# Optimization experiments

Hardware: AMD Instinct MI355X
Metric: run time of the kernel (lower is better)

Reference implementation:

```python
import jax, jax.numpy as jnp
import numpy as np

E = 512      # embed_dim
H = 8        # num_heads
HD = E // H  # head_dim
TGT = 512
SRC = 2048
B = 16


def setup_inputs() -> dict:
    key = jax.random.key(0)
    ks = jax.random.split(key, 10)
    inp = {
        "query": jax.random.normal(ks[0], (TGT, B, E), dtype=jnp.float32),
        "key": jax.random.normal(ks[1], (SRC, B, E), dtype=jnp.float32),
        "value": jax.random.normal(ks[2], (SRC, B, E), dtype=jnp.float32),
        "in_proj_weight": jax.random.normal(ks[3], (3 * E, E), dtype=jnp.float32) * 0.02,
        "in_proj_bias": jax.random.normal(ks[4], (3 * E,), dtype=jnp.float32) * 0.02,
        "bias_k": jax.random.normal(ks[5], (1, 1, E), dtype=jnp.float32) * 0.02,
        "bias_v": jax.random.normal(ks[6], (1, 1, E), dtype=jnp.float32) * 0.02,
        "out_proj_weight": jax.random.normal(ks[7], (E, E), dtype=jnp.float32) * 0.02,
        "out_proj_bias": jnp.zeros((E,), dtype=jnp.float32),
        "key_padding_mask": jax.random.randint(ks[8], (B, SRC), 0, 2).astype(bool),
    }
    return inp


def reference(query, key, value, in_proj_weight, in_proj_bias, bias_k, bias_v,
              out_proj_weight, out_proj_bias, key_padding_mask):
    tgt_len, bsz, embed_dim = query.shape
    scaling = float(HD) ** -0.5

    # manual in-projection (query != key, key is value -> separate q, fused kv)
    q = query @ in_proj_weight[:E].T + in_proj_bias[:E]
    k = key @ in_proj_weight[E:2 * E].T + in_proj_bias[E:2 * E]
    v = value @ in_proj_weight[2 * E:].T + in_proj_bias[2 * E:]
    q = q * scaling

    # bias_k / bias_v concatenation along src dim; pad key_padding_mask with False
    k = jnp.concatenate([k, jnp.broadcast_to(bias_k, (1, bsz, E))], axis=0)
    v = jnp.concatenate([v, jnp.broadcast_to(bias_v, (1, bsz, E))], axis=0)
    kpm = jnp.pad(key_padding_mask, ((0, 0), (0, 1)))  # [B, SRC+1]

    src_len = k.shape[0]
    # [len, B, E] -> [B*H, len, HD]
    q = q.reshape(tgt_len, bsz * H, HD).transpose(1, 0, 2)
    k = k.reshape(src_len, bsz * H, HD).transpose(1, 0, 2)
    v = v.reshape(src_len, bsz * H, HD).transpose(1, 0, 2)

    scores = jnp.einsum('bth,bsh->bts', q, k)  # [B*H, TGT, SRC+1]
    mask = kpm[:, None, None, :]               # [B, 1, 1, SRC+1]
    scores = scores.reshape(bsz, H, tgt_len, src_len)
    scores = jnp.where(mask, -jnp.inf, scores).reshape(bsz * H, tgt_len, src_len)
    attn = jax.nn.softmax(scores, axis=-1)

    out = jnp.einsum('bts,bsh->bth', attn, v)                 # [B*H, TGT, HD]
    out = out.transpose(1, 0, 2).reshape(tgt_len, bsz, E)     # [TGT, B, E]
    out = out @ out_proj_weight.T + out_proj_bias
    return out, attn
```

## Files before the change

### kernel.cpp

```cpp
#include <hip/hip_runtime.h>

#define E    512
#define H    8
#define HD   64
#define TGT  512
#define SRC  2048
#define S1   2049
#define S1P  2112
#define NB   16
#define BH   128
#define NCH  33
#define PW   2120

typedef __attribute__((ext_vector_type(8))) short short8;
typedef __attribute__((ext_vector_type(4))) float floatx4;

__device__ __forceinline__ unsigned short f2bf(float x) {
    unsigned u = __float_as_uint(x);
    u = (u + 0x7FFF + ((u >> 16) & 1)) >> 16;
    return (unsigned short)u;
}

__global__ __launch_bounds__(256) void cvt_bf16(const float* __restrict__ src,
    unsigned short* __restrict__ dst, const int n8)
{
    const int i = blockIdx.x * 256 + threadIdx.x;
    if (i >= n8) return;
    const float4 f0 = ((const float4*)src)[(size_t)i * 2];
    const float4 f1 = ((const float4*)src)[(size_t)i * 2 + 1];
    unsigned short o[8] = {f2bf(f0.x), f2bf(f0.y), f2bf(f0.z), f2bf(f0.w),
                           f2bf(f1.x), f2bf(f1.y), f2bf(f1.z), f2bf(f1.w)};
    ((int4*)dst)[i] = *(int4*)o;
}

__global__ __launch_bounds__(256) void proj_gemm(const unsigned short* __restrict__ X,
    const unsigned short* __restrict__ W, const float* __restrict__ bias,
    unsigned short* __restrict__ Y, const int ld, const float scale)
{
    __shared__ __align__(16) unsigned short As[128][72];
    __shared__ __align__(16) unsigned short Bs[64][72];
    const int tid  = threadIdx.x;
    const int c0   = blockIdx.x << 6;
    const int r0   = blockIdx.y << 7;
    const int w    = tid >> 6, lane = tid & 63, c = lane & 15, quad = lane >> 4;
    floatx4 acc[2][4] = {};
    for (int k0 = 0; k0 < E; k0 += 64) {
#pragma unroll
        for (int i = 0; i < 4; ++i) {
            const int idx = tid + (i << 8);
            const int r = idx >> 3, q = (idx & 7) << 3;
            *(int4*)&As[r][q] = *(const int4*)&X[(size_t)(r0 + r) * E + k0 + q];
        }
#pragma unroll
        for (int i = 0; i < 2; ++i) {
            const int idx = tid + (i << 8);
            const int r = idx >> 3, q = (idx & 7) << 3;
            *(int4*)&Bs[r][q] = *(const int4*)&W[(size_t)(c0 + r) * E + k0 + q];
        }
        __syncthreads();
#pragma unroll
        for (int kh = 0; kh < 2; ++kh) {
            short8 a0 = *(const short8*)&As[(w << 5) + c][(kh << 5) + (quad << 3)];
            short8 a1 = *(const short8*)&As[(w << 5) + 16 + c][(kh << 5) + (quad << 3)];
#pragma unroll
            for (int n = 0; n < 4; ++n) {
                short8 b = *(const short8*)&Bs[(n << 4) + c][(kh << 5) + (quad << 3)];
                acc[0][n] = __builtin_amdgcn_mfma_f32_16x16x32_bf16(a0, b, acc[0][n], 0, 0, 0);
                acc[1][n] = __builtin_amdgcn_mfma_f32_16x16x32_bf16(a1, b, acc[1][n], 0, 0, 0);
            }
        }
        __syncthreads();
    }
#pragma unroll
    for (int mt = 0; mt < 2; ++mt) {
#pragma unroll
        for (int reg = 0; reg < 4; ++reg) {
            const int rg = r0 + (w << 5) + (mt << 4) + (quad << 2) + reg;
            const int t = rg >> 4, b = rg & 15;
#pragma unroll
            for (int n = 0; n < 4; ++n) {
                const int col = c0 + (n << 4) + c;
                const int h = col >> 6, hd = col & 63;
                const float v = (acc[mt][n][reg] + bias[col]) * scale;
                Y[((size_t)(b * H + h) * ld + t) * HD + hd] = f2bf(v);
            }
        }
    }
}

__global__ void fill_bias(const float* __restrict__ bk, const float* __restrict__ bv,
                          unsigned short* __restrict__ kbuf, unsigned short* __restrict__ vtbuf)
{
    const int idx = blockIdx.x * 256 + threadIdx.x;
    const int bh = idx >> 6, hd = idx & 63, h = bh & 7;
    kbuf[((size_t)bh * S1P + SRC) * HD + hd] = f2bf(bk[h * HD + hd]);
    vtbuf[((size_t)bh * HD + hd) * S1P + SRC] = f2bf(bv[h * HD + hd]);
    for (int s = SRC + 1; s < S1P; ++s) {
        kbuf[((size_t)bh * S1P + s) * HD + hd] = 0;
        vtbuf[((size_t)bh * HD + hd) * S1P + s] = 0;
    }
}

__global__ __launch_bounds__(256) void transpose_v(const unsigned short* __restrict__ vbuf,
    unsigned short* __restrict__ vtbuf)
{
    __shared__ __align__(16) unsigned short T[64][72];
    const int tid = threadIdx.x;
    const int s0  = blockIdx.x << 6;
    const int bh  = blockIdx.y;
#pragma unroll
    for (int i = 0; i < 2; ++i) {
        const int idx = tid + (i << 8);
        const int s = idx >> 3, q = (idx & 7) << 3;
        *(int4*)&T[s][q] = *(const int4*)&vbuf[((size_t)bh * SRC + s0 + s) * HD + q];
    }
    __syncthreads();
#pragma unroll
    for (int i = 0; i < 2; ++i) {
        const int idx = tid + (i << 8);
        const int hd = idx >> 3, sq = (idx & 7) << 3;
        unsigned short tmp[8];
#pragma unroll
        for (int j = 0; j < 8; ++j) tmp[j] = T[sq + j][hd];
        *(int4*)&vtbuf[((size_t)bh * HD + hd) * S1P + s0 + sq] = *(int4*)tmp;
    }
}

__global__ __launch_bounds__(256, 2) void attn_fused(
    const unsigned short* __restrict__ qbh,
    const unsigned short* __restrict__ kbuf,
    const unsigned short* __restrict__ vtbuf,
    const int* __restrict__ kpm,
    float* __restrict__ attn, unsigned short* __restrict__ ctx)
{
    __shared__ __align__(16) unsigned short P[16][PW];
    __shared__ float mf[S1P];
    __shared__ float sums[4][16];
    __shared__ float linv[16];
    const int tid = threadIdx.x;
    const int t0  = blockIdx.x << 4;
    const int bh  = blockIdx.y;
    const int bb  = bh >> 3;
    const int w = tid >> 6, lane = tid & 63, c = lane & 15, quad = lane >> 4;

    for (int s = tid; s < S1P; s += 256)
        mf[s] = (s < SRC) ? (kpm[bb * SRC + s] ? 3e38f : 0.f)
                          : ((s == SRC) ? 0.f : 3e38f);

    const unsigned short* qr = &qbh[((size_t)bh * TGT + t0 + c) * HD + (quad << 3)];
    short8 qa0 = *(const short8*)qr;
    short8 qa1 = *(const short8*)(qr + 32);

    __syncthreads();

    float rs[4] = {0.f, 0.f, 0.f, 0.f};
    for (int ch = w; ch < NCH; ch += 4) {
        const int s0 = ch << 6;
        floatx4 sc[4] = {};
#pragma unroll
        for (int n = 0; n < 4; ++n) {
            const unsigned short* kr =
                &kbuf[((size_t)bh * S1P + s0 + (n << 4) + c) * HD + (quad << 3)];
            short8 b0 = *(const short8*)kr;
            short8 b1 = *(const short8*)(kr + 32);
            sc[n] = __builtin_amdgcn_mfma_f32_16x16x32_bf16(qa0, b0, sc[n], 0, 0, 0);
            sc[n] = __builtin_amdgcn_mfma_f32_16x16x32_bf16(qa1, b1, sc[n], 0, 0, 0);
        }
#pragma unroll
        for (int n = 0; n < 4; ++n) {
            const float m = mf[s0 + (n << 4) + c];
#pragma unroll
            for (int reg = 0; reg < 4; ++reg) {
                const float p = __expf(sc[n][reg] - m);
                rs[reg] += p;
                P[(quad << 2) + reg][s0 + (n << 4) + c] = f2bf(p);
            }
        }
    }

#pragma unroll
    for (int reg = 0; reg < 4; ++reg) {
        float v = rs[reg];
        v += __shfl_xor(v, 1); v += __shfl_xor(v, 2);
        v += __shfl_xor(v, 4); v += __shfl_xor(v, 8);
        rs[reg] = v;
    }
    if (c == 0) {
#pragma unroll
        for (int reg = 0; reg < 4; ++reg)
            sums[w][(quad << 2) + reg] = rs[reg];
    }
    __syncthreads();
    if (tid < 16)
        linv[tid] = 1.0f / (sums[0][tid] + sums[1][tid] + sums[2][tid] + sums[3][tid]);
    __syncthreads();

    floatx4 ca = {};
#pragma unroll 6
    for (int kc = 0; kc < 66; ++kc) {
        short8 a = *(const short8*)&P[c][(kc << 5) + (quad << 3)];
        short8 b = *(const short8*)&vtbuf[((size_t)bh * HD + (w << 4) + c) * S1P
                                          + (kc << 5) + (quad << 3)];
        ca = __builtin_amdgcn_mfma_f32_16x16x32_bf16(a, b, ca, 0, 0, 0);
    }
#pragma unroll
    for (int reg = 0; reg < 4; ++reg) {
        const int t = t0 + (quad << 2) + reg;
        ctx[((size_t)bh * TGT + t) * HD + (w << 4) + c] =
            f2bf(ca[reg] * linv[(quad << 2) + reg]);
    }

    for (int ch = w; ch < NCH; ch += 4) {
        const int s0 = ch << 6;
        if (ch < 32) {
#pragma unroll
            for (int r = 0; r < 16; ++r) {
                const float p =
                    __uint_as_float((unsigned)P[r][s0 + lane] << 16) * linv[r];
                attn[((size_t)bh * TGT + t0 + r) * S1 + s0 + lane] = p;
            }
        } else if (lane < 16) {
            const float p =
                __uint_as_float((unsigned)P[lane][2048] << 16) * linv[lane];
            attn[((size_t)bh * TGT + t0 + lane) * S1 + 2048] = p;
        }
    }
}

__global__ __launch_bounds__(256) void outproj_gemm(const unsigned short* __restrict__ ctx,
    const unsigned short* __restrict__ W, const float* __restrict__ bias,
    float* __restrict__ out)
{
    __shared__ __align__(16) unsigned short As[128][72];
    __shared__ __align__(16) unsigned short Bs[64][72];
    const int tid = threadIdx.x;
    const int c0  = blockIdx.x << 6;
    const int r0  = blockIdx.y << 7;
    const int w   = tid >> 6, lane = tid & 63, c = lane & 15, quad = lane >> 4;
    floatx4 acc[2][4] = {};
    for (int k0 = 0; k0 < E; k0 += 64) {
        const int h = k0 >> 6;
#pragma unroll
        for (int i = 0; i < 4; ++i) {
            const int idx = tid + (i << 8);
            const int r = idx >> 3, q = (idx & 7) << 3;
            const int rg = r0 + r, t = rg >> 4, b = rg & 15;
            *(int4*)&As[r][q] = *(const int4*)&ctx[((size_t)(b * H + h) * TGT + t) * HD + q];
        }
#pragma unroll
        for (int i = 0; i < 2; ++i) {
            const int idx = tid + (i << 8);
            const int r = idx >> 3, q = (idx & 7) << 3;
            *(int4*)&Bs[r][q] = *(const int4*)&W[(size_t)(c0 + r) * E + k0 + q];
        }
        __syncthreads();
#pragma unroll
        for (int kh = 0; kh < 2; ++kh) {
            short8 a0 = *(const short8*)&As[(w << 5) + c][(kh << 5) + (quad << 3)];
            short8 a1 = *(const short8*)&As[(w << 5) + 16 + c][(kh << 5) + (quad << 3)];
#pragma unroll
            for (int n = 0; n < 4; ++n) {
                short8 b = *(const short8*)&Bs[(n << 4) + c][(kh << 5) + (quad << 3)];
                acc[0][n] = __builtin_amdgcn_mfma_f32_16x16x32_bf16(a0, b, acc[0][n], 0, 0, 0);
                acc[1][n] = __builtin_amdgcn_mfma_f32_16x16x32_bf16(a1, b, acc[1][n], 0, 0, 0);
            }
        }
        __syncthreads();
    }
#pragma unroll
    for (int mt = 0; mt < 2; ++mt) {
#pragma unroll
        for (int reg = 0; reg < 4; ++reg) {
            const int rg = r0 + (w << 5) + (mt << 4) + (quad << 2) + reg;
#pragma unroll
            for (int n = 0; n < 4; ++n) {
                const int col = c0 + (n << 4) + c;
                out[(size_t)rg * E + col] = acc[mt][n][reg] + bias[col];
            }
        }
    }
}

extern "C" void kernel_launch(void* const* d_in, const int* in_sizes, int n_in,
                              void* d_out, int out_size, void* d_ws, size_t ws_size,
                              hipStream_t stream)
{
    const float* query  = (const float*)d_in[0];
    const float* key    = (const float*)d_in[1];
    const float* value  = (const float*)d_in[2];
    const float* ipw    = (const float*)d_in[3];
    const float* ipb    = (const float*)d_in[4];
    const float* bias_k = (const float*)d_in[5];
    const float* bias_v = (const float*)d_in[6];
    const float* opw    = (const float*)d_in[7];
    const float* opb    = (const float*)d_in[8];
    const int*   kpm    = (const int*)d_in[9];

    float* out  = (float*)d_out;
    float* attn = out + (size_t)TGT * NB * E;

    unsigned short* k_bf = (unsigned short*)attn;
    unsigned short* v_bf = k_bf + (size_t)16777216;
    unsigned short* vbuf = v_bf + (size_t)16777216;

    char* ws = (char*)d_ws;
    unsigned short* q_bf  = (unsigned short*)ws;
    unsigned short* wi_bf = q_bf  + (size_t)4194304;
    unsigned short* wo_bf = wi_bf + (size_t)786432;
    unsigned short* qbh   = wo_bf + (size_t)262144;
    unsigned short* kbuf  = qbh   + (size_t)4194304;
    unsigned short* vtbuf = kbuf  + (size_t)17301504;
    unsigned short* ctx   = vtbuf + (size_t)17301504;

    cvt_bf16<<<dim3(2048), 256, 0, stream>>>(query, q_bf, 524288);
    cvt_bf16<<<dim3(8192), 256, 0, stream>>>(key,   k_bf, 2097152);
    cvt_bf16<<<dim3(8192), 256, 0, stream>>>(value, v_bf, 2097152);
    cvt_bf16<<<dim3(384),  256, 0, stream>>>(ipw,   wi_bf, 98304);
    cvt_bf16<<<dim3(128),  256, 0, stream>>>(opw,   wo_bf, 32768);

    proj_gemm<<<dim3(8, 64),  256, 0, stream>>>(q_bf, wi_bf,          ipb,         qbh,  TGT, 0.125f);
    proj_gemm<<<dim3(8, 256), 256, 0, stream>>>(k_bf, wi_bf + 262144, ipb + E,     kbuf, S1P, 1.0f);
    proj_gemm<<<dim3(8, 256), 256, 0, stream>>>(v_bf, wi_bf + 524288, ipb + 2 * E, vbuf, SRC, 1.0f);

    fill_bias<<<dim3(32), 256, 0, stream>>>(bias_k, bias_v, kbuf, vtbuf);
    transpose_v<<<dim3(32, 128), 256, 0, stream>>>(vbuf, vtbuf);

    attn_fused<<<dim3(32, 128), 256, 0, stream>>>(qbh, kbuf, vtbuf, kpm, attn, ctx);
    outproj_gemm<<<dim3(8, 64), 256, 0, stream>>>(ctx, wo_bf, opb, out);
}
```

Baseline: 1.106 ms.

## Software-pipeline K/V loads and overlap attn stores with PV MFMA

The QK loop now double-buffers K fragments in registers, loading the next chunk while the current one is computed. The PV loop is restructured to 64-wide steps with two accumulators and prefetched V fragments. The attention-probability stores, previously a separate pass, are interleaved into the PV loop and use nontemporal stores, as is the ctx write. The aim is to hide global-load latency and overlap the large attn write with MFMA work, at the cost of higher register pressure.

```diff
diff --git a/kernel.cpp b/kernel.cpp
--- a/kernel.cpp
+++ b/kernel.cpp
@@ -151,32 +151,51 @@
     short8 qa0 = *(const short8*)qr;
     short8 qa1 = *(const short8*)(qr + 32);
 
+#define LOADK(D0, D1, CH) do {                                                  \
+        const unsigned short* kb_ = &kbuf[((size_t)bh * S1P + ((CH) << 6)) * HD]; \
+        _Pragma("unroll")                                                       \
+        for (int n_ = 0; n_ < 4; ++n_) {                                        \
+            const unsigned short* kr_ = kb_ + ((n_ << 4) + c) * HD + (quad << 3); \
+            D0[n_] = *(const short8*)kr_;                                       \
+            D1[n_] = *(const short8*)(kr_ + 32);                                \
+        }                                                                       \
+    } while (0)
+
+#define QK_COMPUTE(CH, B0, B1) do {                                             \
+        const int s0_ = (CH) << 6;                                              \
+        floatx4 sc_[4] = {};                                                    \
+        _Pragma("unroll")                                                       \
+        for (int n_ = 0; n_ < 4; ++n_) {                                        \
+            sc_[n_] = __builtin_amdgcn_mfma_f32_16x16x32_bf16(qa0, B0[n_], sc_[n_], 0, 0, 0); \
+            sc_[n_] = __builtin_amdgcn_mfma_f32_16x16x32_bf16(qa1, B1[n_], sc_[n_], 0, 0, 0); \
+        }                                                                       \
+        _Pragma("unroll")                                                       \
+        for (int n_ = 0; n_ < 4; ++n_) {                                        \
+            const float m_ = mf[s0_ + (n_ << 4) + c];                           \
+            _Pragma("unroll")                                                   \
+            for (int rg_ = 0; rg_ < 4; ++rg_) {                                 \
+                const float p_ = __expf(sc_[n_][rg_] - m_);                     \
+                rs[rg_] += p_;                                                  \
+                P[(quad << 2) + rg_][s0_ + (n_ << 4) + c] = f2bf(p_);           \
+            }                                                                   \
+        }                                                                       \
+    } while (0)
+
+    short8 kb0[4], kb1[4];
+    LOADK(kb0, kb1, w);
+
     __syncthreads();
 
     float rs[4] = {0.f, 0.f, 0.f, 0.f};
-    for (int ch = w; ch < NCH; ch += 4) {
-        const int s0 = ch << 6;
-        floatx4 sc[4] = {};
-#pragma unroll
-        for (int n = 0; n < 4; ++n) {
-            const unsigned short* kr =
-                &kbuf[((size_t)bh * S1P + s0 + (n << 4) + c) * HD + (quad << 3)];
-            short8 b0 = *(const short8*)kr;
-            short8 b1 = *(const short8*)(kr + 32);
-            sc[n] = __builtin_amdgcn_mfma_f32_16x16x32_bf16(qa0, b0, sc[n], 0, 0, 0);
-            sc[n] = __builtin_amdgcn_mfma_f32_16x16x32_bf16(qa1, b1, sc[n], 0, 0, 0);
-        }
-#pragma unroll
-        for (int n = 0; n < 4; ++n) {
-            const float m = mf[s0 + (n << 4) + c];
-#pragma unroll
-            for (int reg = 0; reg < 4; ++reg) {
-                const float p = __expf(sc[n][reg] - m);
-                rs[reg] += p;
-                P[(quad << 2) + reg][s0 + (n << 4) + c] = f2bf(p);
-            }
-        }
-    }
+    int ch;
+    for (ch = w; ch + 4 < NCH; ch += 4) {
+        short8 nb0[4], nb1[4];
+        LOADK(nb0, nb1, ch + 4);
+        QK_COMPUTE(ch, kb0, kb1);
+#pragma unroll
+        for (int n = 0; n < 4; ++n) { kb0[n] = nb0[n]; kb1[n] = nb1[n]; }
+    }
+    QK_COMPUTE(ch, kb0, kb1);
 
 #pragma unroll
     for (int reg = 0; reg < 4; ++reg) {
@@ -195,36 +214,56 @@
         linv[tid] = 1.0f / (sums[0][tid] + sums[1][tid] + sums[2][tid] + sums[3][tid]);
     __syncthreads();
 
-    floatx4 ca = {};
-#pragma unroll 6
-    for (int kc = 0; kc < 66; ++kc) {
-        short8 a = *(const short8*)&P[c][(kc << 5) + (quad << 3)];
-        short8 b = *(const short8*)&vtbuf[((size_t)bh * HD + (w << 4) + c) * S1P
-                                          + (kc << 5) + (quad << 3)];
-        ca = __builtin_amdgcn_mfma_f32_16x16x32_bf16(a, b, ca, 0, 0, 0);
-    }
+#define STORE_CHUNK(CH) do {                                                    \
+        if ((CH) < 32) {                                                        \
+            _Pragma("unroll")                                                   \
+            for (int r_ = 0; r_ < 16; ++r_) {                                   \
+                const float p_ = __uint_as_float(                               \
+                    (unsigned)P[r_][((CH) << 6) + lane] << 16) * linv[r_];      \
+                __builtin_nontemporal_store(p_,                                 \
+                    &attn[((size_t)bh * TGT + t0 + r_) * S1 + ((CH) << 6) + lane]); \
+            }                                                                   \
+        } else if (lane < 16) {                                                 \
+            const float p_ = __uint_as_float(                                   \
+                (unsigned)P[lane][2048] << 16) * linv[lane];                    \
+            __builtin_nontemporal_store(p_,                                     \
+                &attn[((size_t)bh * TGT + t0 + lane) * S1 + 2048]);             \
+        }                                                                       \
+    } while (0)
+
+    const unsigned short* vrow = &vtbuf[((size_t)bh * HD + (w << 4) + c) * S1P];
+    floatx4 ca0 = {}, ca1 = {};
+    short8 vb0 = *(const short8*)&vrow[(quad << 3)];
+    short8 vb1 = *(const short8*)&vrow[32 + (quad << 3)];
+#pragma unroll 4
+    for (int kc = 0; kc < 32; ++kc) {
+        short8 nv0 = *(const short8*)&vrow[((kc + 1) << 6) + (quad << 3)];
+        short8 nv1 = *(const short8*)&vrow[((kc + 1) << 6) + 32 + (quad << 3)];
+        short8 a0 = *(const short8*)&P[c][(kc << 6) + (quad << 3)];
+        short8 a1 = *(const short8*)&P[c][(kc << 6) + 32 + (quad << 3)];
+        ca0 = __builtin_amdgcn_mfma_f32_16x16x32_bf16(a0, vb0, ca0, 0, 0, 0);
+        ca1 = __builtin_amdgcn_mfma_f32_16x16x32_bf16(a1, vb1, ca1, 0, 0, 0);
+        if ((kc & 3) == w) STORE_CHUNK(kc);
+        vb0 = nv0; vb1 = nv1;
+    }
+    {
+        short8 a0 = *(const short8*)&P[c][(32 << 6) + (quad << 3)];
+        short8 a1 = *(const short8*)&P[c][(32 << 6) + 32 + (quad << 3)];
+        ca0 = __builtin_amdgcn_mfma_f32_16x16x32_bf16(a0, vb0, ca0, 0, 0, 0);
+        ca1 = __builtin_amdgcn_mfma_f32_16x16x32_bf16(a1, vb1, ca1, 0, 0, 0);
+        if (w == 0) STORE_CHUNK(32);
+    }
+
 #pragma unroll
     for (int reg = 0; reg < 4; ++reg) {
         const int t = t0 + (quad << 2) + reg;
-        ctx[((size_t)bh * TGT + t) * HD + (w << 4) + c] =
-            f2bf(ca[reg] * linv[(quad << 2) + reg]);
-    }
-
-    for (int ch = w; ch < NCH; ch += 4) {
-        const int s0 = ch << 6;
-        if (ch < 32) {
-#pragma unroll
-            for (int r = 0; r < 16; ++r) {
-                const float p =
-                    __uint_as_float((unsigned)P[r][s0 + lane] << 16) * linv[r];
-                attn[((size_t)bh * TGT + t0 + r) * S1 + s0 + lane] = p;
-            }
-        } else if (lane < 16) {
-            const float p =
-                __uint_as_float((unsigned)P[lane][2048] << 16) * linv[lane];
-            attn[((size_t)bh * TGT + t0 + lane) * S1 + 2048] = p;
-        }
-    }
+        const float v = (ca0[reg] + ca1[reg]) * linv[(quad << 2) + reg];
+        __builtin_nontemporal_store(f2bf(v),
+            &ctx[((size_t)bh * TGT + t) * HD + (w << 4) + c]);
+    }
+#undef LOADK
+#undef QK_COMPUTE
+#undef STORE_CHUNK
 }
 
 __global__ __launch_bounds__(256) void outproj_gemm(const unsigned short* __restrict__ ctx,
```

New measurement: 1.094 ms. Within noise of the previous version (-1.1%).

## Widen attention block to 8 waves with prefetched K and split PV reduction

Applied to the files above, without the earlier changes.

The fused attention kernel now runs 512 threads per block. The QK loop software-prefetches the next K chunk and its mask values into registers, replacing the shared-memory mask table. The PV product is split across two halves of the source dimension and combined through shared memory, using two accumulators to raise MFMA independence. fill_bias is also rewritten to parallelise the zero-padding writes over many threads with vectorised stores. The launch bounds of (512,4) and the larger shared footprint may limit occupancy or force register spills.

```diff
diff --git a/kernel.cpp b/kernel.cpp
--- a/kernel.cpp
+++ b/kernel.cpp
@@ -88,15 +88,27 @@
     }
 }
 
-__global__ void fill_bias(const float* __restrict__ bk, const float* __restrict__ bv,
-                          unsigned short* __restrict__ kbuf, unsigned short* __restrict__ vtbuf)
+#define FB_BIAS  8192
+#define FB_KPAD  64512
+#define FB_VPAD  516096
+__global__ __launch_bounds__(256) void fill_bias(const float* __restrict__ bk,
+    const float* __restrict__ bv,
+    unsigned short* __restrict__ kbuf, unsigned short* __restrict__ vtbuf)
 {
     const int idx = blockIdx.x * 256 + threadIdx.x;
-    const int bh = idx >> 6, hd = idx & 63, h = bh & 7;
-    kbuf[((size_t)bh * S1P + SRC) * HD + hd] = f2bf(bk[h * HD + hd]);
-    vtbuf[((size_t)bh * HD + hd) * S1P + SRC] = f2bf(bv[h * HD + hd]);
-    for (int s = SRC + 1; s < S1P; ++s) {
-        kbuf[((size_t)bh * S1P + s) * HD + hd] = 0;
+    if (idx < FB_BIAS) {
+        const int bh = idx >> 6, hd = idx & 63, h = bh & 7;
+        kbuf[((size_t)bh * S1P + SRC) * HD + hd] = f2bf(bk[h * HD + hd]);
+        vtbuf[((size_t)bh * HD + hd) * S1P + SRC] = f2bf(bv[h * HD + hd]);
+    } else if (idx < FB_BIAS + FB_KPAD) {
+        const int i = idx - FB_BIAS;
+        const int bh = i / 504, o = i % 504;
+        const int4 z = {0, 0, 0, 0};
+        ((int4*)&kbuf[((size_t)bh * S1P + S1) * HD])[o] = z;
+    } else if (idx < FB_BIAS + FB_KPAD + FB_VPAD) {
+        const int i = idx - FB_BIAS - FB_KPAD;
+        const int bh = i / 4032, r = i % 4032;
+        const int hd = r / 63, s = S1 + r % 63;
         vtbuf[((size_t)bh * HD + hd) * S1P + s] = 0;
     }
 }
@@ -126,7 +138,7 @@
     }
 }
 
-__global__ __launch_bounds__(256, 2) void attn_fused(
+__global__ __launch_bounds__(512, 4) void attn_fused(
     const unsigned short* __restrict__ qbh,
     const unsigned short* __restrict__ kbuf,
     const unsigned short* __restrict__ vtbuf,
@@ -134,8 +146,8 @@
     float* __restrict__ attn, unsigned short* __restrict__ ctx)
 {
     __shared__ __align__(16) unsigned short P[16][PW];
-    __shared__ float mf[S1P];
-    __shared__ float sums[4][16];
+    __shared__ float cpart[16][68];
+    __shared__ float sums[8][16];
     __shared__ float linv[16];
     const int tid = threadIdx.x;
     const int t0  = blockIdx.x << 4;
@@ -143,40 +155,59 @@
     const int bb  = bh >> 3;
     const int w = tid >> 6, lane = tid & 63, c = lane & 15, quad = lane >> 4;
 
-    for (int s = tid; s < S1P; s += 256)
-        mf[s] = (s < SRC) ? (kpm[bb * SRC + s] ? 3e38f : 0.f)
-                          : ((s == SRC) ? 0.f : 3e38f);
-
     const unsigned short* qr = &qbh[((size_t)bh * TGT + t0 + c) * HD + (quad << 3)];
     short8 qa0 = *(const short8*)qr;
     short8 qa1 = *(const short8*)(qr + 32);
 
-    __syncthreads();
+#define LOADK(D0, D1, M, CH) do {                                               \
+        const unsigned short* kb_ = &kbuf[((size_t)bh * S1P + ((CH) << 6)) * HD]; \
+        _Pragma("unroll")                                                       \
+        for (int n_ = 0; n_ < 4; ++n_) {                                        \
+            const unsigned short* kr_ = kb_ + ((n_ << 4) + c) * HD + (quad << 3); \
+            D0[n_] = *(const short8*)kr_;                                       \
+            D1[n_] = *(const short8*)(kr_ + 32);                                \
+        }                                                                       \
+        _Pragma("unroll")                                                       \
+        for (int n_ = 0; n_ < 4; ++n_) {                                        \
+            const int s_ = ((CH) << 6) + (n_ << 4) + c;                         \
+            M[n_] = (s_ < SRC) ? (kpm[bb * SRC + s_] ? 3e38f : 0.f)             \
+                               : ((s_ == SRC) ? 0.f : 3e38f);                   \
+        }                                                                       \
+    } while (0)
+
+#define QK_COMPUTE(CH, B0, B1, M) do {                                          \
+        const int s0_ = (CH) << 6;                                              \
+        floatx4 sc_[4] = {};                                                    \
+        _Pragma("unroll")                                                       \
+        for (int n_ = 0; n_ < 4; ++n_) {                                        \
+            sc_[n_] = __builtin_amdgcn_mfma_f32_16x16x32_bf16(qa0, B0[n_], sc_[n_], 0, 0, 0); \
+            sc_[n_] = __builtin_amdgcn_mfma_f32_16x16x32_bf16(qa1, B1[n_], sc_[n_], 0, 0, 0); \
+        }                                                                       \
+        _Pragma("unroll")                                                       \
+        for (int n_ = 0; n_ < 4; ++n_) {                                        \
+            _Pragma("unroll")                                                   \
+            for (int rg_ = 0; rg_ < 4; ++rg_) {                                 \
+                const float p_ = __expf(sc_[n_][rg_] - M[n_]);                  \
+                rs[rg_] += p_;                                                  \
+                P[(quad << 2) + rg_][s0_ + (n_ << 4) + c] = f2bf(p_);           \
+            }                                                                   \
+        }                                                                       \
+    } while (0)
 
     float rs[4] = {0.f, 0.f, 0.f, 0.f};
-    for (int ch = w; ch < NCH; ch += 4) {
-        const int s0 = ch << 6;
-        floatx4 sc[4] = {};
-#pragma unroll
-        for (int n = 0; n < 4; ++n) {
-            const unsigned short* kr =
-                &kbuf[((size_t)bh * S1P + s0 + (n << 4) + c) * HD + (quad << 3)];
-            short8 b0 = *(const short8*)kr;
-            short8 b1 = *(const short8*)(kr + 32);
-            sc[n] = __builtin_amdgcn_mfma_f32_16x16x32_bf16(qa0, b0, sc[n], 0, 0, 0);
-            sc[n] = __builtin_amdgcn_mfma_f32_16x16x32_bf16(qa1, b1, sc[n], 0, 0, 0);
-        }
-#pragma unroll
-        for (int n = 0; n < 4; ++n) {
-            const float m = mf[s0 + (n << 4) + c];
-#pragma unroll
-            for (int reg = 0; reg < 4; ++reg) {
-                const float p = __expf(sc[n][reg] - m);
-                rs[reg] += p;
-                P[(quad << 2) + reg][s0 + (n << 4) + c] = f2bf(p);
-            }
-        }
-    }
+    short8 kb0[4], kb1[4];
+    float mk[4];
+    LOADK(kb0, kb1, mk, w);
+    int ch;
+    for (ch = w; ch + 8 < NCH; ch += 8) {
+        short8 nb0[4], nb1[4];
+        float nm[4];
+        LOADK(nb0, nb1, nm, ch + 8);
+        QK_COMPUTE(ch, kb0, kb1, mk);
+#pragma unroll
+        for (int n = 0; n < 4; ++n) { kb0[n] = nb0[n]; kb1[n] = nb1[n]; mk[n] = nm[n]; }
+    }
+    QK_COMPUTE(ch, kb0, kb1, mk);
 
 #pragma unroll
     for (int reg = 0; reg < 4; ++reg) {
@@ -191,28 +222,51 @@
             sums[w][(quad << 2) + reg] = rs[reg];
     }
     __syncthreads();
-    if (tid < 16)
-        linv[tid] = 1.0f / (sums[0][tid] + sums[1][tid] + sums[2][tid] + sums[3][tid]);
+    if (tid < 16) {
+        float s = 0.f;
+#pragma unroll
+        for (int i = 0; i < 8; ++i) s += sums[i][tid];
+        linv[tid] = 1.0f / s;
+    }
     __syncthreads();
 
-    floatx4 ca = {};
-#pragma unroll 6
-    for (int kc = 0; kc < 66; ++kc) {
-        short8 a = *(const short8*)&P[c][(kc << 5) + (quad << 3)];
-        short8 b = *(const short8*)&vtbuf[((size_t)bh * HD + (w << 4) + c) * S1P
-                                          + (kc << 5) + (quad << 3)];
-        ca = __builtin_amdgcn_mfma_f32_16x16x32_bf16(a, b, ca, 0, 0, 0);
-    }
-#pragma unroll
-    for (int reg = 0; reg < 4; ++reg) {
-        const int t = t0 + (quad << 2) + reg;
-        ctx[((size_t)bh * TGT + t) * HD + (w << 4) + c] =
-            f2bf(ca[reg] * linv[(quad << 2) + reg]);
-    }
-
-    for (int ch = w; ch < NCH; ch += 4) {
-        const int s0 = ch << 6;
-        if (ch < 32) {
+    const int hs = w & 3, kh2 = w >> 2;
+    const int base = kh2 * 1056;
+    const unsigned short* vrow = &vtbuf[((size_t)bh * HD + (hs << 4) + c) * S1P + base];
+    const unsigned short* prow = &P[c][base];
+    floatx4 ca0 = {}, ca1 = {};
+#pragma unroll 4
+    for (int kc = 0; kc < 16; ++kc) {
+        short8 a0 = *(const short8*)&prow[(kc << 6) + (quad << 3)];
+        short8 a1 = *(const short8*)&prow[(kc << 6) + 32 + (quad << 3)];
+        short8 b0 = *(const short8*)&vrow[(kc << 6) + (quad << 3)];
+        short8 b1 = *(const short8*)&vrow[(kc << 6) + 32 + (quad << 3)];
+        ca0 = __builtin_amdgcn_mfma_f32_16x16x32_bf16(a0, b0, ca0, 0, 0, 0);
+        ca1 = __builtin_amdgcn_mfma_f32_16x16x32_bf16(a1, b1, ca1, 0, 0, 0);
+    }
+    {
+        short8 a = *(const short8*)&prow[1024 + (quad << 3)];
+        short8 b = *(const short8*)&vrow[1024 + (quad << 3)];
+        ca0 = __builtin_amdgcn_mfma_f32_16x16x32_bf16(a, b, ca0, 0, 0, 0);
+    }
+    if (kh2 == 1) {
+#pragma unroll
+        for (int reg = 0; reg < 4; ++reg)
+            cpart[(quad << 2) + reg][(hs << 4) + c] = ca0[reg] + ca1[reg];
+    }
+    __syncthreads();
+    if (kh2 == 0) {
+#pragma unroll
+        for (int reg = 0; reg < 4; ++reg) {
+            const int row = (quad << 2) + reg;
+            const float v = (ca0[reg] + ca1[reg] + cpart[row][(hs << 4) + c]) * linv[row];
+            ctx[((size_t)bh * TGT + t0 + row) * HD + (hs << 4) + c] = f2bf(v);
+        }
+    }
+
+    for (int c2 = w; c2 < NCH; c2 += 8) {
+        const int s0 = c2 << 6;
+        if (c2 < 32) {
 #pragma unroll
             for (int r = 0; r < 16; ++r) {
                 const float p =
@@ -225,6 +279,8 @@
             attn[((size_t)bh * TGT + t0 + lane) * S1 + 2048] = p;
         }
     }
+#undef LOADK
+#undef QK_COMPUTE
 }
 
 __global__ __launch_bounds__(256) void outproj_gemm(const unsigned short* __restrict__ ctx,
@@ -322,9 +378,9 @@
     proj_gemm<<<dim3(8, 256), 256, 0, stream>>>(k_bf, wi_bf + 262144, ipb + E,     kbuf, S1P, 1.0f);
     proj_gemm<<<dim3(8, 256), 256, 0, stream>>>(v_bf, wi_bf + 524288, ipb + 2 * E, vbuf, SRC, 1.0f);
 
-    fill_bias<<<dim3(32), 256, 0, stream>>>(bias_k, bias_v, kbuf, vtbuf);
+    fill_bias<<<dim3(2300), 256, 0, stream>>>(bias_k, bias_v, kbuf, vtbuf);
     transpose_v<<<dim3(32, 128), 256, 0, stream>>>(vbuf, vtbuf);
 
-    attn_fused<<<dim3(32, 128), 256, 0, stream>>>(qbh, kbuf, vtbuf, kpm, attn, ctx);
+    attn_fused<<<dim3(32, 128), 512, 0, stream>>>(qbh, kbuf, vtbuf, kpm, attn, ctx);
     outproj_gemm<<<dim3(8, 64), 256, 0, stream>>>(ctx, wo_bf, opb, out);
 }
```

After: 1.083 ms. 2.1% less time.
